# Performance work log

Hardware: AMD Instinct MI355X
Metric: run time of the kernel (lower is better)

## Reference

```python
import jax, jax.numpy as jnp
import numpy as np
import math

EPS = 1e-5        # matches module-level EPS used to normalize loc
K_PROP = 16       # proposals per element for Wood's rejection sampler (accept rate >>0.5 for m=5)


def _log_ive_1p5(x):
    """log of exponentially-scaled modified Bessel I_{3/2}(x)*exp(-x), closed form for half-integer order.
    I_{3/2}(x) = sqrt(2/(pi x)) * (cosh(x) - sinh(x)/x);  with the exp(-x) scaling
    cosh(x)e^{-x} = (1+e^{-2x})/2 and sinh(x)e^{-x} = (1-e^{-2x})/2."""
    em2 = jnp.exp(-2.0 * x)
    val = jnp.sqrt(2.0 / (jnp.pi * x)) * ((1.0 + em2) * 0.5 - (1.0 - em2) / (2.0 * x))
    return jnp.log(val)


def _vmf_forward(kappa_mu, n_samples, key):
    B, V, m = kappa_mu.shape            # m = vmf_dim + 1 (must be 5 for the closed-form Bessel)
    scale = jnp.linalg.norm(kappa_mu, axis=2, keepdims=True)     # [B,V,1] = kappa
    loc = kappa_mu / (scale + EPS)                               # [B,V,m] unit mean direction

    # --- Wood's rejection sampling constants (as in hyperspherical_vae VonMisesFisher) ---
    c = jnp.sqrt(4.0 * scale ** 2 + (m - 1) ** 2)
    b_true = (-2.0 * scale + c) / (m - 1)
    b_app = (m - 1) / (4.0 * scale)
    s = jnp.clip(scale - 10.0, 0.0, 1.0)          # smooth switch to Taylor approx for large kappa
    b = b_app * s + b_true * (1.0 - s)
    a = (m - 1 + 2.0 * scale + c) / 4.0
    d = (4.0 * a * b) / (1.0 + b) - (m - 1) * math.log(m - 1)

    kb, ku, kv = jax.random.split(key, 3)
    con = (m - 1) / 2.0
    prop_shape = (n_samples, B, V, 1, K_PROP)
    e = jax.random.beta(kb, con, con, prop_shape)                          # Beta proposals
    u = jax.random.uniform(ku, prop_shape, minval=1e-20, maxval=1.0 - 1e-20)
    bb = b[None, ..., None]
    aa = a[None, ..., None]
    dd = d[None, ..., None]
    denom = 1.0 - (1.0 - bb) * e
    w_prop = (1.0 - (1.0 + bb) * e) / denom
    t = (2.0 * aa * bb) / denom
    accept = ((m - 1.0) * jnp.log(t) - t + dd) > jnp.log(u)               # [n,B,V,1,K]
    idx = jnp.argmax(accept, axis=-1)                                      # first accepted proposal
    w = jnp.take_along_axis(w_prop, idx[..., None], axis=-1)[..., 0]       # [n,B,V,1]

    # --- tangent direction + concatenate to sphere point ---
    v = jax.random.normal(kv, (n_samples, B, V, m - 1))
    v = v / jnp.linalg.norm(v, axis=-1, keepdims=True)
    w_ = jnp.sqrt(jnp.clip(1.0 - w ** 2, 1e-10))
    x = jnp.concatenate([w, w_ * v], axis=-1)                              # [n,B,V,m]

    # --- Householder rotation mapping e1 -> loc ---
    e1 = jnp.zeros((m,), dtype=kappa_mu.dtype).at[0].set(1.0)
    uvec = e1 - loc
    uvec = uvec / (jnp.linalg.norm(uvec, axis=-1, keepdims=True) + 1e-5)
    z = x - 2.0 * jnp.sum(x * uvec, axis=-1, keepdims=True) * uvec         # [n,B,V,m]

    # --- log prob under each vMF, summed over the product factors ---
    sc = scale[..., 0]                                                     # [B,V]
    log_unnorm = jnp.sum(loc * z, axis=-1) * sc                            # [n,B,V]
    log_norm = -((m / 2 - 1) * jnp.log(sc) - (m / 2) * math.log(2 * math.pi)
                 - (sc + _log_ive_1p5(sc)))                                 # [B,V]
    log_prob = jnp.sum(log_unnorm - log_norm, axis=-1)                     # [n,B]

    samples = z.reshape(n_samples, B, V * m)                               # [n,B,z_dim]
    return samples.transpose(1, 0, 2), log_prob.transpose(1, 0)            # [B,n,z_dim], [B,n]


def setup_inputs() -> dict:
    key = jax.random.key(0)
    B, V, m = 2048, 64, 5
    kappa_mu = jax.random.normal(key, (B, V, m), dtype=jnp.float32)
    return {"kappa_mu": kappa_mu, "n_samples": 16}


def reference(kappa_mu, n_samples):
    key = jax.random.key(1)
    samples, log_prob = _vmf_forward(kappa_mu, n_samples, key)
    return samples, log_prob
```

## Files before the change

kernel.cpp:

```cpp
#include <hip/hip_runtime.h>
#include <stdint.h>
#include <math.h>

#pragma clang fp contract(off)

struct U2 { uint32_t x, y; };

__host__ __device__ constexpr U2 tf(uint32_t k0, uint32_t k1, uint32_t x0, uint32_t x1) {
  uint32_t k2 = k0 ^ k1 ^ 0x1BD11BDAu;
#define TF_R(r) { x0 += x1; x1 = (x1 << (r)) | (x1 >> (32 - (r))); x1 ^= x0; }
  x0 += k0; x1 += k1;
  TF_R(13) TF_R(15) TF_R(26) TF_R(6)
  x0 += k1; x1 += k2 + 1u;
  TF_R(17) TF_R(29) TF_R(16) TF_R(24)
  x0 += k2; x1 += k0 + 2u;
  TF_R(13) TF_R(15) TF_R(26) TF_R(6)
  x0 += k0; x1 += k1 + 3u;
  TF_R(17) TF_R(29) TF_R(16) TF_R(24)
  x0 += k1; x1 += k2 + 4u;
  TF_R(13) TF_R(15) TF_R(26) TF_R(6)
  x0 += k2; x1 += k0 + 5u;
#undef TF_R
  return U2{x0, x1};
}

__device__ constexpr U2 T0 = tf(0u, 1u, 0u, 0u);
__device__ constexpr U2 T1 = tf(0u, 1u, 0u, 1u);
__device__ constexpr U2 T2 = tf(0u, 1u, 0u, 2u);
__device__ constexpr U2 KA = tf(T0.x, T0.y, 0u, 0u);
__device__ constexpr U2 KB = tf(T0.x, T0.y, 0u, 1u);

__device__ __forceinline__ U2 srow(U2 k, uint32_t i) { return tf(k.x, k.y, 0u, i); }
__device__ __forceinline__ uint32_t rb(U2 k, uint32_t i) {
  U2 r = tf(k.x, k.y, 0u, i); return r.x ^ r.y;
}

__device__ __forceinline__ float u01f(uint32_t b) {
  return __uint_as_float((b >> 9) | 0x3F800000u) - 1.0f;
}

__device__ float log_x(float a) {
  if (a == 0.0f) return -__builtin_inff();
  if (a < 0.0f) return __builtin_nanf("");
  if (__builtin_isinf(a)) return a;
  uint32_t bits = __float_as_uint(a);
  int e = (int)(bits >> 23) - 126;
  float m = __uint_as_float((bits & 0x007FFFFFu) | 0x3F000000u);
  if (m < 0.70710678118654752440f) { e -= 1; m = m + m - 1.0f; }
  else                             { m = m - 1.0f; }
  float z = m * m;
  float y = fmaf(7.0376836292E-2f, m, -1.1514610310E-1f);
  y = fmaf(y, m,  1.1676998740E-1f);
  y = fmaf(y, m, -1.2420140846E-1f);
  y = fmaf(y, m,  1.4249322787E-1f);
  y = fmaf(y, m, -1.6668057665E-1f);
  y = fmaf(y, m,  2.0000714765E-1f);
  y = fmaf(y, m, -2.4999993993E-1f);
  y = fmaf(y, m,  3.3333331174E-1f);
  y = y * m; y = y * z;
  y = fmaf((float)e, -2.12194440e-4f, y);
  y = fmaf(z, -0.5f, y);
  float r = m + y;
  r = fmaf((float)e, 0.693359375f, r);
  return r;
}

__device__ float exp_x(float a) {
  float x = fminf(a, 88.3762626647950f);
  x = fmaxf(x, -88.3762626647949f);
  float fx = floorf(fmaf(x, 1.44269504088896341f, 0.5f));
  x = x - fx * 0.693359375f;
  x = x - fx * (-2.12194440e-4f);
  float z = x * x;
  float y = fmaf(1.9875691500E-4f, x, 1.3981999507E-3f);
  y = fmaf(y, x, 8.3334519073E-3f);
  y = fmaf(y, x, 4.1665795894E-2f);
  y = fmaf(y, x, 1.6666665459E-1f);
  y = fmaf(y, x, 5.0000001201E-1f);
  y = fmaf(y, z, x);
  y = y + 1.0f;
  return ldexpf(y, (int)fx);
}

__device__ __forceinline__ float log1p_x(float x) {
  float u = 1.0f + x;
  if (u == 1.0f) return x;
  return x * (log_x(u) / (u - 1.0f));
}

__device__ float erfinv_x(float x) {
  float w = -log1p_x(-(x * x));
  float p;
  if (w < 5.0f) {
    w = w - 2.5f;
    p = 2.81022636e-08f;
    p = p * w + 3.43273939e-07f;
    p = p * w + (-3.5233877e-06f);
    p = p * w + (-4.39150654e-06f);
    p = p * w + 0.00021858087f;
    p = p * w + (-0.00125372503f);
    p = p * w + (-0.00417768164f);
    p = p * w + 0.246640727f;
    p = p * w + 1.50140941f;
  } else {
    w = sqrtf(w) - 3.0f;
    p = -0.000200214257f;
    p = p * w + 0.000100950558f;
    p = p * w + 0.00134934322f;
    p = p * w + (-0.00367342844f);
    p = p * w + 0.00573950773f;
    p = p * w + (-0.0076224613f);
    p = p * w + 0.00943887047f;
    p = p * w + 1.00167406f;
    p = p * w + 2.83297682f;
  }
  return p * x;
}

#define F_NEG_ALMOST1 (-0.99999994039535522f)
#define F_SQRT2       (1.4142135623730951f)

#define NB   2048
#define NS   16
#define NV   64
#define ZDIM 320
#define SAMPLES_ELEMS (2048ull*16ull*320ull)

__global__ __launch_bounds__(256) void vmf_kernel(const float* __restrict__ km,
                                                  float* __restrict__ out) {
  const int tid  = threadIdx.x;
  const int wd   = tid >> 6;
  const int lane = tid & 63;
  const int bs   = blockIdx.x * 4 + wd;
  const int b    = bs >> 4;
  const int s    = bs & 15;
  const int vv   = lane;

  const float Dg = 2.0f - 0.33333334f;
  const float Cg = 0.33333334f * (1.0f / sqrtf(Dg));
  const float logDg = log_x(Dg);

  const float* kp = km + ((size_t)b * NV + vv) * 5;
  float m0 = kp[0], m1 = kp[1], m2 = kp[2], m3 = kp[3], m4 = kp[4];
  float kap = sqrtf(m0*m0 + m1*m1 + m2*m2 + m3*m3 + m4*m4);
  float l0 = m0 / (kap + 1e-5f);
  float l1 = m1 / (kap + 1e-5f);
  float l2 = m2 / (kap + 1e-5f);
  float l3 = m3 / (kap + 1e-5f);
  float l4 = m4 / (kap + 1e-5f);

  float cw = sqrtf(4.0f * (kap * kap) + 16.0f);
  float b_true = (-2.0f * kap + cw) / 4.0f;
  float b_app  = 4.0f / (4.0f * kap);
  float ssw = fminf(fmaxf(kap - 10.0f, 0.0f), 1.0f);
  float bw = b_app * ssw + b_true * (1.0f - ssw);
  float aw = (4.0f + 2.0f * kap + cw) / 4.0f;
  float dw = (4.0f * aw * bw) / (1.0f + bw) - 5.545177444479562f;

  const uint32_t site = ((uint32_t)(s * NB + b) * NV + (uint32_t)vv);

  float w = 0.0f, w0 = 0.0f, lga = 0.0f;
  int kprop = 0;
  bool phaseB = false;
  bool done = false;
  uint32_t i = site * 16u;
  U2 k = srow(srow(KA, i), 0u);

  #pragma unroll 1
  for (int it = 0; it < 3200; ++it) {
    if (__all(done)) break;
    if (!done) {
      U2 xk = srow(k, 1u);
      U2 Uk = srow(k, 2u);
      U2 sub = srow(xk, 1u);
      float f = u01f(rb(sub, 0u));
      float un = fmaxf(F_NEG_ALMOST1, f * 2.0f + F_NEG_ALMOST1);
      float x = F_SQRT2 * erfinv_x(un);
      float v = 1.0f + x * Cg;
      if (v <= 0.0f) {
        U2 chain = srow(xk, 0u);
        #pragma unroll 1
        for (int r = 0; r < 16 && v <= 0.0f; ++r) {
          U2 sk = srow(chain, 1u);
          chain = srow(chain, 0u);
          float f2 = u01f(rb(sk, 0u));
          float un2 = fmaxf(F_NEG_ALMOST1, f2 * 2.0f + F_NEG_ALMOST1);
          x = F_SQRT2 * erfinv_x(un2);
          v = 1.0f + x * Cg;
        }
      }
      float X = x * x;
      float V = (v * v) * v;
      float lV = log_x(V);
      float U = u01f(rb(Uk, 0u));
      bool c1 = U >= (1.0f - 0.0331f * (X * X));
      bool c2 = log_x(U) >= (X * 0.5f + Dg * ((1.0f - V) + lV));
      if (c1 && c2) {
        k = srow(k, 0u);
      } else {
        float lg = logDg + lV;
        if (!phaseB) {
          lga = lg;
          phaseB = true;
          k = srow(srow(KB, i), 0u);
        } else {
          float lgb = lg;
          float lm = fmaxf(lga, lgb);
          float ea = exp_x(lga - lm);
          float eb = exp_x(lgb - lm);
          float e = ea / (ea + eb);
          float fu = u01f(rb(T1, i));
          float uu = fmaxf(1e-20f, fu * 1.0f + 1e-20f);
          float denom = 1.0f - (1.0f - bw) * e;
          float wp = (1.0f - (1.0f + bw) * e) / denom;
          float tt = (2.0f * aw * bw) / denom;
          float st = 4.0f * log_x(tt) - tt + dw;
          bool acc = st > log_x(uu);
          if (kprop == 0) w0 = wp;
          if (acc) { w = wp; done = true; }
          else {
            ++kprop;
            if (kprop == 16) { w = w0; done = true; }
            else {
              ++i; phaseB = false;
              k = srow(srow(KA, i), 0u);
            }
          }
        }
      }
    }
  }

  uint32_t j0 = site * 4u;
  float f, un, n0, n1, n2, n3;
  f = u01f(rb(T2, j0 + 0u)); un = fmaxf(F_NEG_ALMOST1, f*2.0f + F_NEG_ALMOST1); n0 = F_SQRT2*erfinv_x(un);
  f = u01f(rb(T2, j0 + 1u)); un = fmaxf(F_NEG_ALMOST1, f*2.0f + F_NEG_ALMOST1); n1 = F_SQRT2*erfinv_x(un);
  f = u01f(rb(T2, j0 + 2u)); un = fmaxf(F_NEG_ALMOST1, f*2.0f + F_NEG_ALMOST1); n2 = F_SQRT2*erfinv_x(un);
  f = u01f(rb(T2, j0 + 3u)); un = fmaxf(F_NEG_ALMOST1, f*2.0f + F_NEG_ALMOST1); n3 = F_SQRT2*erfinv_x(un);
  float nn = sqrtf(n0*n0 + n1*n1 + n2*n2 + n3*n3);
  n0 /= nn; n1 /= nn; n2 /= nn; n3 /= nn;

  float w_ = sqrtf(fmaxf(1.0f - w * w, 1e-10f));
  float x0 = w, x1 = w_ * n0, x2 = w_ * n1, x3 = w_ * n2, x4 = w_ * n3;

  float u0 = 1.0f - l0, u1 = -l1, u2 = -l2, u3 = -l3, u4 = -l4;
  float un_ = sqrtf(u0*u0 + u1*u1 + u2*u2 + u3*u3 + u4*u4);
  u0 /= (un_ + 1e-5f); u1 /= (un_ + 1e-5f); u2 /= (un_ + 1e-5f);
  u3 /= (un_ + 1e-5f); u4 /= (un_ + 1e-5f);
  float dot = x0*u0 + x1*u1 + x2*u2 + x3*u3 + x4*u4;
  float z0 = x0 - (2.0f * dot) * u0;
  float z1 = x1 - (2.0f * dot) * u1;
  float z2 = x2 - (2.0f * dot) * u2;
  float z3 = x3 - (2.0f * dot) * u3;
  float z4 = x4 - (2.0f * dot) * u4;

  float* zo = out + (size_t)(b * NS + s) * ZDIM + (size_t)vv * 5;
  zo[0] = z0; zo[1] = z1; zo[2] = z2; zo[3] = z3; zo[4] = z4;

  float dlz = l0*z0 + l1*z1 + l2*z2 + l3*z3 + l4*z4;
  float lu = dlz * kap;
  float em2 = exp_x(-2.0f * kap);
  float val = sqrtf(2.0f / (3.14159274f * kap)) *
              ((1.0f + em2) * 0.5f - (1.0f - em2) / (2.0f * kap));
  float li = log_x(val);
  float term = lu + ((1.5f * log_x(kap) - 4.594692666023363f) - (kap + li));

  float acc = term;
  #pragma unroll
  for (int off = 1; off < 64; off <<= 1) acc += __shfl_xor(acc, off, 64);
  if (lane == 0) out[SAMPLES_ELEMS + (size_t)(b * NS + s)] = acc;
}

extern "C" void kernel_launch(void* const* d_in, const int* in_sizes, int n_in,
                              void* d_out, int out_size, void* d_ws, size_t ws_size,
                              hipStream_t stream) {
  const float* km = (const float*)d_in[0];
  float* out = (float*)d_out;
  hipLaunchKernelGGL(vmf_kernel, dim3(32768 / 4), dim3(256), 0, stream, km, out);
}
```

Before: 244.1 us.

## Split rejection sampling into persistent per-thread site queue kernel plus finish kernel

The rejection-sampling loop moves into its own kernel where each thread processes 16 sites back to back, picking up a new site as soon as the current one finishes. This targets wavefront divergence, where the whole wave used to wait for its slowest lane. A second kernel reads the sampled w from the output buffer and does the tangent, reflection and log-prob work. The cost is an extra launch, a round trip of w through global memory, and scattered writes of w from the first kernel.

```diff
diff --git a/kernel.cpp b/kernel.cpp
--- a/kernel.cpp
+++ b/kernel.cpp
@@ -125,51 +125,49 @@
 #define NV   64
 #define ZDIM 320
 #define SAMPLES_ELEMS (2048ull*16ull*320ull)
-
-__global__ __launch_bounds__(256) void vmf_kernel(const float* __restrict__ km,
-                                                  float* __restrict__ out) {
-  const int tid  = threadIdx.x;
-  const int wd   = tid >> 6;
-  const int lane = tid & 63;
-  const int bs   = blockIdx.x * 4 + wd;
-  const int b    = bs >> 4;
-  const int s    = bs & 15;
-  const int vv   = lane;
+#define NSITES (2048u*16u*64u)
+#define T_SITES 16u
+#define A_THREADS (NSITES / T_SITES)
+
+__global__ __launch_bounds__(256) void sample_w(const float* __restrict__ km,
+                                                float* __restrict__ out) {
+  const uint32_t gtid = blockIdx.x * 256u + threadIdx.x;
 
   const float Dg = 2.0f - 0.33333334f;
   const float Cg = 0.33333334f * (1.0f / sqrtf(Dg));
   const float logDg = log_x(Dg);
 
-  const float* kp = km + ((size_t)b * NV + vv) * 5;
-  float m0 = kp[0], m1 = kp[1], m2 = kp[2], m3 = kp[3], m4 = kp[4];
-  float kap = sqrtf(m0*m0 + m1*m1 + m2*m2 + m3*m3 + m4*m4);
-  float l0 = m0 / (kap + 1e-5f);
-  float l1 = m1 / (kap + 1e-5f);
-  float l2 = m2 / (kap + 1e-5f);
-  float l3 = m3 / (kap + 1e-5f);
-  float l4 = m4 / (kap + 1e-5f);
-
-  float cw = sqrtf(4.0f * (kap * kap) + 16.0f);
-  float b_true = (-2.0f * kap + cw) / 4.0f;
-  float b_app  = 4.0f / (4.0f * kap);
-  float ssw = fminf(fmaxf(kap - 10.0f, 0.0f), 1.0f);
-  float bw = b_app * ssw + b_true * (1.0f - ssw);
-  float aw = (4.0f + 2.0f * kap + cw) / 4.0f;
-  float dw = (4.0f * aw * bw) / (1.0f + bw) - 5.545177444479562f;
-
-  const uint32_t site = ((uint32_t)(s * NB + b) * NV + (uint32_t)vv);
-
-  float w = 0.0f, w0 = 0.0f, lga = 0.0f;
+  uint32_t t = 0;
+  bool need_init = true;
+  uint32_t site = 0, i = 0;
   int kprop = 0;
   bool phaseB = false;
-  bool done = false;
-  uint32_t i = site * 16u;
-  U2 k = srow(srow(KA, i), 0u);
+  U2 k = {0u, 0u};
+  float bw = 0.f, aw = 0.f, dw = 0.f, w0 = 0.f, lga = 0.f;
 
   #pragma unroll 1
-  for (int it = 0; it < 3200; ++it) {
-    if (__all(done)) break;
-    if (!done) {
+  for (int it = 0; it < 60000; ++it) {
+    if (__all(t >= T_SITES)) break;
+    bool active = (t < T_SITES);
+    if (active && need_init) {
+      site = gtid * T_SITES + t;
+      uint32_t bv = site & (NB * NV - 1u);
+      const float* kp = km + (size_t)bv * 5u;
+      float m0 = kp[0], m1 = kp[1], m2 = kp[2], m3 = kp[3], m4 = kp[4];
+      float kap = sqrtf(m0*m0 + m1*m1 + m2*m2 + m3*m3 + m4*m4);
+      float cwv = sqrtf(4.0f * (kap * kap) + 16.0f);
+      float b_true = (-2.0f * kap + cwv) / 4.0f;
+      float b_app  = 4.0f / (4.0f * kap);
+      float ssw = fminf(fmaxf(kap - 10.0f, 0.0f), 1.0f);
+      bw = b_app * ssw + b_true * (1.0f - ssw);
+      aw = (4.0f + 2.0f * kap + cwv) / 4.0f;
+      dw = (4.0f * aw * bw) / (1.0f + bw) - 5.545177444479562f;
+      i = site * 16u;
+      kprop = 0; phaseB = false;
+      k = srow(srow(KA, i), 0u);
+      need_init = false;
+    }
+    if (active) {
       U2 xk = srow(k, 1u);
       U2 Uk = srow(k, 2u);
       U2 sub = srow(xk, 1u);
@@ -199,6 +197,8 @@
         k = srow(k, 0u);
       } else {
         float lg = logDg + lV;
+        bool finish = false;
+        float wres = 0.0f;
         if (!phaseB) {
           lga = lg;
           phaseB = true;
@@ -217,20 +217,50 @@
           float st = 4.0f * log_x(tt) - tt + dw;
           bool acc = st > log_x(uu);
           if (kprop == 0) w0 = wp;
-          if (acc) { w = wp; done = true; }
+          if (acc) { wres = wp; finish = true; }
           else {
             ++kprop;
-            if (kprop == 16) { w = w0; done = true; }
-            else {
-              ++i; phaseB = false;
-              k = srow(srow(KA, i), 0u);
-            }
+            if (kprop == 16) { wres = w0; finish = true; }
+            else { ++i; phaseB = false; k = srow(srow(KA, i), 0u); }
           }
+        }
+        if (finish) {
+          uint32_t vv = site & (NV - 1u);
+          uint32_t sb = site >> 6;
+          uint32_t s  = sb >> 11;
+          uint32_t b  = sb & (NB - 1u);
+          out[(size_t)(b * NS + s) * ZDIM + (size_t)vv * 5u] = wres;
+          ++t;
+          need_init = true;
         }
       }
     }
   }
-
+}
+
+__global__ __launch_bounds__(256) void vmf_finish(const float* __restrict__ km,
+                                                  float* __restrict__ out) {
+  const int tid  = threadIdx.x;
+  const int wd   = tid >> 6;
+  const int lane = tid & 63;
+  const int bs   = blockIdx.x * 4 + wd;
+  const int b    = bs >> 4;
+  const int s    = bs & 15;
+  const int vv   = lane;
+
+  const float* kp = km + ((size_t)b * NV + vv) * 5;
+  float m0 = kp[0], m1 = kp[1], m2 = kp[2], m3 = kp[3], m4 = kp[4];
+  float kap = sqrtf(m0*m0 + m1*m1 + m2*m2 + m3*m3 + m4*m4);
+  float l0 = m0 / (kap + 1e-5f);
+  float l1 = m1 / (kap + 1e-5f);
+  float l2 = m2 / (kap + 1e-5f);
+  float l3 = m3 / (kap + 1e-5f);
+  float l4 = m4 / (kap + 1e-5f);
+
+  float* zo = out + (size_t)(b * NS + s) * ZDIM + (size_t)vv * 5;
+  float w = zo[0];
+
+  const uint32_t site = ((uint32_t)(s * NB + b) * NV + (uint32_t)vv);
   uint32_t j0 = site * 4u;
   float f, un, n0, n1, n2, n3;
   f = u01f(rb(T2, j0 + 0u)); un = fmaxf(F_NEG_ALMOST1, f*2.0f + F_NEG_ALMOST1); n0 = F_SQRT2*erfinv_x(un);
@@ -254,7 +284,6 @@
   float z3 = x3 - (2.0f * dot) * u3;
   float z4 = x4 - (2.0f * dot) * u4;
 
-  float* zo = out + (size_t)(b * NS + s) * ZDIM + (size_t)vv * 5;
   zo[0] = z0; zo[1] = z1; zo[2] = z2; zo[3] = z3; zo[4] = z4;
 
   float dlz = l0*z0 + l1*z1 + l2*z2 + l3*z3 + l4*z4;
@@ -276,5 +305,6 @@
                               hipStream_t stream) {
   const float* km = (const float*)d_in[0];
   float* out = (float*)d_out;
-  hipLaunchKernelGGL(vmf_kernel, dim3(32768 / 4), dim3(256), 0, stream, km, out);
-}
+  hipLaunchKernelGGL(sample_w,   dim3(A_THREADS / 256), dim3(256), 0, stream, km, out);
+  hipLaunchKernelGGL(vmf_finish, dim3(32768 / 4),       dim3(256), 0, stream, km, out);
+}
```

Result: no change. 246.5 us (+1.0%).
